# Kernel optimization log

Hardware: AMD Instinct MI355X
Metric: run time of the kernel (lower is better)

## Reference

```python
import jax, jax.numpy as jnp
import numpy as np
from jax import lax

WINDOW_SIZE = 11
SIGMA = 1.5
RGB_RANGE = 1.0
K1, K2 = 0.01, 0.03
CHANNELS = 3


def gaussian_window(window_size, sigma, channels, dtype=jnp.float32):
    coords = jnp.arange(window_size, dtype=dtype) - window_size // 2
    g = jnp.exp(-(coords ** 2) / (2.0 * sigma * sigma))
    g = g / g.sum()
    w2d = jnp.outer(g, g)
    w2d = w2d / w2d.sum()
    # depthwise kernel: (C, 1, ws, ws) in OIHW with feature_group_count=C
    return jnp.broadcast_to(w2d, (channels, 1, window_size, window_size)).astype(dtype)


def _dwconv(inp, window, padding):
    # depthwise conv2d, groups = C
    C = inp.shape[1]
    return lax.conv_general_dilated(
        inp, window,
        window_strides=(1, 1),
        padding=[(padding, padding), (padding, padding)],
        feature_group_count=C,
        dimension_numbers=('NCHW', 'OIHW', 'NCHW'))


def setup_inputs() -> dict:
    key = jax.random.key(0)
    kx, ky = jax.random.split(key)
    B, C, H, W = 16, CHANNELS, 512, 512
    x = jax.random.uniform(kx, (B, C, H, W), dtype=jnp.float32)
    y = jax.random.uniform(ky, (B, C, H, W), dtype=jnp.float32)
    window = gaussian_window(WINDOW_SIZE, SIGMA, C)
    return {"x": x, "y": y, "window": window}


def reference(x, y, window):
    padding = WINDOW_SIZE // 2
    mu_x = _dwconv(x, window, padding)
    mu_y = _dwconv(y, window, padding)
    mu_x2 = mu_x * mu_x
    mu_y2 = mu_y * mu_y
    mu_xy = mu_x * mu_y
    sigma_x2 = _dwconv(x * x, window, padding) - mu_x2
    sigma_y2 = _dwconv(y * y, window, padding) - mu_y2
    sigma_xy = _dwconv(x * y, window, padding) - mu_xy
    L = RGB_RANGE
    C1 = (K1 * L) ** 2
    C2 = (K2 * L) ** 2
    ssim_map = ((2.0 * mu_xy + C1) * (2.0 * sigma_xy + C2)) / (
        (mu_x2 + mu_y2 + C1) * (sigma_x2 + sigma_y2 + C2) + 1e-12)
    loss = 1.0 - ssim_map
    return loss.mean()
```

## Files before the change

kernel.cpp:

```cpp
#include <hip/hip_runtime.h>


typedef __fp16 f16x8 __attribute__((ext_vector_type(8)));
typedef float f32x4 __attribute__((ext_vector_type(4)));
typedef unsigned u32x4 __attribute__((ext_vector_type(4)));

__device__ __forceinline__ unsigned pk2(float a, float b) {
    return __builtin_bit_cast(unsigned, __builtin_amdgcn_cvt_pkrtz(a, b));
}
__device__ __forceinline__ f32x4 mfma16(f16x8 a, f16x8 b, f32x4 c) {
    return __builtin_amdgcn_mfma_f32_16x16x32_f16(a, b, c, 0, 0, 0);
}

#define SXW 24
#define HRP 40

__global__ __launch_bounds__(512, 8) void ssim_main(
    const float* __restrict__ xg, const float* __restrict__ yg,
    const float* __restrict__ w2d, float* __restrict__ part)
{
    __shared__ __align__(16) unsigned sx[80 * SXW];
    __shared__ __align__(16) unsigned sy[80 * SXW];
    __shared__ __align__(16) unsigned hq[2][32 * HRP];
    __shared__ unsigned tbp[64];
    __shared__ float gsf[12];
    __shared__ float wred[8];

    const int tid = threadIdx.x;

    if (tid < 12) {
        float s = 0.0f;
        if (tid < 11) {
            #pragma unroll
            for (int j = 0; j < 11; ++j) s += w2d[tid * 11 + j];
        }
        gsf[tid] = s;
    }

    const int nwg = 128 * (int)gridDim.z;
    const int flat = (int)blockIdx.x + 16 * ((int)blockIdx.y + 8 * (int)blockIdx.z);
    const int swz = (flat & 7) * (nwg >> 3) + (flat >> 3);
    const int bx = swz & 15, by = (swz >> 4) & 7, bz = swz >> 7;

    const int x0 = bx * 32 - 8;
    const int y0 = by * 64 - 9;
    const size_t zoff = (size_t)bz * (512 * 512);
    const float* __restrict__ xp = xg + zoff;
    const float* __restrict__ yp = yg + zoff;

    const bool interior = (x0 >= 0) & (x0 + 47 < 512) & (y0 >= 0) & (y0 + 79 < 512);
    if (interior) {
        for (int it = tid; it < 80 * 12; it += 512) {
            const int r = it / 12, c4 = it - r * 12;
            const int o = (y0 + r) * 512 + x0 + 4 * c4;
            const float4 vx = *(const float4*)&xp[o];
            const float4 vy = *(const float4*)&yp[o];
            *(uint2*)&sx[2 * it] = make_uint2(pk2(vx.x, vx.y), pk2(vx.z, vx.w));
            *(uint2*)&sy[2 * it] = make_uint2(pk2(vy.x, vy.y), pk2(vy.z, vy.w));
        }
    } else {
        for (int it = tid; it < 80 * 12; it += 512) {
            const int r = it / 12, c4 = it - r * 12;
            const int gr = y0 + r, gc0 = x0 + 4 * c4;
            const bool rok = (unsigned)gr < 512u;
            float xv[4], yv[4];
            #pragma unroll
            for (int j = 0; j < 4; ++j) {
                const int gc = gc0 + j;
                const bool ok = rok & ((unsigned)gc < 512u);
                const int o = gr * 512 + gc;
                xv[j] = ok ? xp[o] : 0.f;
                yv[j] = ok ? yp[o] : 0.f;
            }
            *(uint2*)&sx[2 * it] = make_uint2(pk2(xv[0], xv[1]), pk2(xv[2], xv[3]));
            *(uint2*)&sy[2 * it] = make_uint2(pk2(yv[0], yv[1]), pk2(yv[2], yv[3]));
        }
    }
    __syncthreads();

    if (tid < 64) {
        float ssum = 0.0f;
        #pragma unroll
        for (int k = 0; k < 11; ++k)
            if (k != 5) ssum += (float)(__fp16)gsf[k];
        const __fp16 cc = (__fp16)(1.0f - ssum);
        auto tap = [&](int t) -> __fp16 {
            if ((unsigned)t > 10u) return (__fp16)0.f;
            return (t == 5) ? cc : (__fp16)gsf[t];
        };
        const int t = tid - 19;
        const unsigned short lo = __builtin_bit_cast(unsigned short, tap(t));
        const unsigned short hi = __builtin_bit_cast(unsigned short, tap(t + 1));
        tbp[tid] = (unsigned)lo | ((unsigned)hi << 16);
    }
    __syncthreads();

    const int lane = tid & 63, wv = tid >> 6;
    const int lm = lane & 15, lg = lane >> 4;

    f16x8 bt, afr;
    {
        const int k0 = 8 * lg - lm + 16;
        u32x4 wb, wa;
        #pragma unroll
        for (int i = 0; i < 4; ++i) {
            wb[i] = tbp[k0 + 2 * i];
            wa[i] = tbp[k0 - 1 + 2 * i];
        }
        bt  = __builtin_bit_cast(f16x8, wb);
        afr = __builtin_bit_cast(f16x8, wa);
    }

    auto ldpair = [&](int i, f16x8& xa, f16x8& ya) {
        const int b = i >> 1, tl = i & 1;
        const int sbase = (16 * b + lm) * SXW + 8 * tl + 4 * lg;
        xa = __builtin_bit_cast(f16x8, *(const u32x4*)&sx[sbase]);
        ya = __builtin_bit_cast(f16x8, *(const u32x4*)&sy[sbase]);
    };
    f16x8 xa0, ya0;
    ldpair(wv, xa0, ya0);

    f32x4 acc[5];
    #pragma unroll
    for (int q = 0; q < 5; ++q) acc[q] = (f32x4){0.f, 0.f, 0.f, 0.f};

    const int rq = wv >> 1, ch = wv & 1;
    const int rpb = 8 * rq;

    #pragma unroll
    for (int chunk = 0; chunk < 3; ++chunk) {
        auto bitem = [&](const f16x8& xa, const f16x8& ya, int i) {
            const int b = i >> 1, tl = i & 1;
            const f32x4 z4 = {0.f, 0.f, 0.f, 0.f};
            f32x4 d0 = z4, d1 = z4;
            if (chunk == 0)      { d0 = mfma16(xa, bt, z4);      d1 = mfma16(ya, bt, z4); }
            else if (chunk == 1) { d0 = mfma16(xa * xa, bt, z4); d1 = mfma16(ya * ya, bt, z4); }
            else                 { d0 = mfma16(xa * ya, bt, z4); }
            const int ob = (16 * tl + lm) * HRP + 8 * b + 2 * lg;
            *(uint2*)&hq[0][ob] = make_uint2(pk2(d0[0], d0[1]), pk2(d0[2], d0[3]));
            if (chunk < 2)
                *(uint2*)&hq[1][ob] = make_uint2(pk2(d1[0], d1[1]), pk2(d1[2], d1[3]));
        };
        bitem(xa0, ya0, wv);
        if (wv < 2) {
            f16x8 xf, yf;
            ldpair(wv + 8, xf, yf);
            bitem(xf, yf, wv + 8);
        }
        __syncthreads();

        {
            const int cb = (16 * ch + lm) * HRP + rpb + 4 * lg;
            #pragma unroll
            for (int s = 0; s < 2; ++s) {
                if (chunk == 2 && s == 1) continue;
                const u32x4 w4 = *(const u32x4*)&hq[s][cb];
                acc[2 * chunk + s] =
                    mfma16(afr, __builtin_bit_cast(f16x8, w4), acc[2 * chunk + s]);
            }
        }
        if (chunk < 2) __syncthreads();
    }

    float lsum = 0.0f;
    const float C1 = 1e-4f, C2 = 9e-4f;
    #pragma unroll
    for (int r = 0; r < 4; ++r) {
        const float mx = acc[0][r], my = acc[1][r];
        const float exx = acc[2][r], eyy = acc[3][r];
        const float exy = acc[4][r];
        const float mx2 = mx * mx, my2 = my * my, mxy = mx * my;
        const float vx = exx - mx2, vy = eyy - my2, vxy = exy - mxy;
        const float num = (2.0f * mxy + C1) * (2.0f * vxy + C2);
        const float den = (mx2 + my2 + C1) * (vx + vy + C2) + 1e-12f;
        lsum = fmaf(num, __builtin_amdgcn_rcpf(den), lsum);
    }

    #pragma unroll
    for (int off = 32; off > 0; off >>= 1)
        lsum += __shfl_down(lsum, off, 64);
    if ((tid & 63) == 0) wred[tid >> 6] = lsum;
    __syncthreads();
    if (tid == 0) {
        float s = 0.0f;
        #pragma unroll
        for (int w = 0; w < 8; ++w) s += wred[w];
        part[swz] = s;
    }
}

__global__ __launch_bounds__(256) void ssim_reduce(
    const float* __restrict__ part, float* __restrict__ out,
    int n, float invN)
{
    __shared__ float wred[4];
    float s = 0.0f;
    for (int i = threadIdx.x; i < n; i += 256) s += part[i];
    #pragma unroll
    for (int off = 32; off > 0; off >>= 1)
        s += __shfl_down(s, off, 64);
    if ((threadIdx.x & 63) == 0) wred[threadIdx.x >> 6] = s;
    __syncthreads();
    if (threadIdx.x == 0)
        out[0] = 1.0f - (wred[0] + wred[1] + wred[2] + wred[3]) * invN;
}

extern "C" void kernel_launch(void* const* d_in, const int* in_sizes, int n_in,
                              void* d_out, int out_size, void* d_ws, size_t ws_size,
                              hipStream_t stream) {
    const float* x   = (const float*)d_in[0];
    const float* y   = (const float*)d_in[1];
    const float* w2d = (const float*)d_in[2];
    float* out  = (float*)d_out;
    float* part = (float*)d_ws;

    const int H = 512, W = 512;
    const int total = in_sizes[0];
    const int Z = total / (H * W);

    dim3 grid(W / 32, H / 64, Z);
    const int nblk = (W / 32) * (H / 64) * Z;
    ssim_main<<<grid, 512, 0, stream>>>(x, y, w2d, part);

    const float invN = 1.0f / (float)total;
    ssim_reduce<<<1, 256, 0, stream>>>(part, out, nblk, invN);
}
```

Measured before the change: 145.9 us.

## Process two tiles per workgroup with prefetch overlapping global loads and compute

Each workgroup now handles two adjacent 32x64 tiles, halving the grid. The second tile's global loads are issued into registers before the first tile's MFMA phases run, so memory latency overlaps compute. The five horizontal-pass results now go into five LDS buffers, which cuts the per-tile barriers from several chunked rounds to a few. Plain barriers are replaced with an explicit lgkmcnt wait plus s_barrier. In exchange, LDS use rises and the occupancy hint drops from 8 to 6, so fewer workgroups may be resident at once.

```diff
diff --git a/kernel.cpp b/kernel.cpp
--- a/kernel.cpp
+++ b/kernel.cpp
@@ -11,17 +11,20 @@
 __device__ __forceinline__ f32x4 mfma16(f16x8 a, f16x8 b, f32x4 c) {
     return __builtin_amdgcn_mfma_f32_16x16x32_f16(a, b, c, 0, 0, 0);
 }
+__device__ __forceinline__ void ldsBarrier() {
+    asm volatile("s_waitcnt lgkmcnt(0)\n\ts_barrier" ::: "memory");
+}
 
 #define SXW 24
 #define HRP 40
 
-__global__ __launch_bounds__(512, 8) void ssim_main(
+__global__ __launch_bounds__(512, 6) void ssim_main(
     const float* __restrict__ xg, const float* __restrict__ yg,
     const float* __restrict__ w2d, float* __restrict__ part)
 {
     __shared__ __align__(16) unsigned sx[80 * SXW];
     __shared__ __align__(16) unsigned sy[80 * SXW];
-    __shared__ __align__(16) unsigned hq[2][32 * HRP];
+    __shared__ __align__(16) unsigned hq[5][32 * HRP];
     __shared__ unsigned tbp[64];
     __shared__ float gsf[12];
     __shared__ float wred[8];
@@ -37,52 +40,64 @@
         gsf[tid] = s;
     }
 
-    const int nwg = 128 * (int)gridDim.z;
-    const int flat = (int)blockIdx.x + 16 * ((int)blockIdx.y + 8 * (int)blockIdx.z);
-    const int swz = (flat & 7) * (nwg >> 3) + (flat >> 3);
-    const int bx = swz & 15, by = (swz >> 4) & 7, bz = swz >> 7;
-
-    const int x0 = bx * 32 - 8;
-    const int y0 = by * 64 - 9;
-    const size_t zoff = (size_t)bz * (512 * 512);
-    const float* __restrict__ xp = xg + zoff;
-    const float* __restrict__ yp = yg + zoff;
-
-    const bool interior = (x0 >= 0) & (x0 + 47 < 512) & (y0 >= 0) & (y0 + 79 < 512);
-    if (interior) {
-        for (int it = tid; it < 80 * 12; it += 512) {
-            const int r = it / 12, c4 = it - r * 12;
+    const int npair = 64 * (int)gridDim.z;
+    const int flat = (int)blockIdx.x + 8 * ((int)blockIdx.y + 8 * (int)blockIdx.z);
+    const int k = (flat & 7) * (npair >> 3) + (flat >> 3);
+    const int t0 = 2 * k, t1 = 2 * k + 1;
+
+    const int it0 = tid, it1 = tid + 512;
+    const bool has1 = (it1 < 960);
+
+    auto decode = [&](int t, int& x0, int& y0, const float*& xp,
+                      const float*& yp, bool& inter) {
+        const int bx = t & 15, by = (t >> 4) & 7, bz = t >> 7;
+        x0 = bx * 32 - 8;
+        y0 = by * 64 - 9;
+        const size_t zoff = (size_t)bz * (512 * 512);
+        xp = xg + zoff; yp = yg + zoff;
+        inter = (x0 >= 0) & (x0 + 47 < 512) & (y0 >= 0) & (y0 + 79 < 512);
+    };
+    auto loadItem = [&](const float* xp, const float* yp, int x0, int y0,
+                        bool inter, int it, float4& xv, float4& yv) {
+        const int r = it / 12, c4 = it - r * 12;
+        if (inter) {
             const int o = (y0 + r) * 512 + x0 + 4 * c4;
-            const float4 vx = *(const float4*)&xp[o];
-            const float4 vy = *(const float4*)&yp[o];
-            *(uint2*)&sx[2 * it] = make_uint2(pk2(vx.x, vx.y), pk2(vx.z, vx.w));
-            *(uint2*)&sy[2 * it] = make_uint2(pk2(vy.x, vy.y), pk2(vy.z, vy.w));
-        }
-    } else {
-        for (int it = tid; it < 80 * 12; it += 512) {
-            const int r = it / 12, c4 = it - r * 12;
+            xv = *(const float4*)&xp[o];
+            yv = *(const float4*)&yp[o];
+        } else {
             const int gr = y0 + r, gc0 = x0 + 4 * c4;
             const bool rok = (unsigned)gr < 512u;
-            float xv[4], yv[4];
+            float tx[4], ty[4];
             #pragma unroll
             for (int j = 0; j < 4; ++j) {
                 const int gc = gc0 + j;
                 const bool ok = rok & ((unsigned)gc < 512u);
                 const int o = gr * 512 + gc;
-                xv[j] = ok ? xp[o] : 0.f;
-                yv[j] = ok ? yp[o] : 0.f;
+                tx[j] = ok ? xp[o] : 0.f;
+                ty[j] = ok ? yp[o] : 0.f;
             }
-            *(uint2*)&sx[2 * it] = make_uint2(pk2(xv[0], xv[1]), pk2(xv[2], xv[3]));
-            *(uint2*)&sy[2 * it] = make_uint2(pk2(yv[0], yv[1]), pk2(yv[2], yv[3]));
-        }
-    }
-    __syncthreads();
+            xv = make_float4(tx[0], tx[1], tx[2], tx[3]);
+            yv = make_float4(ty[0], ty[1], ty[2], ty[3]);
+        }
+    };
+    auto writeItem = [&](int it, const float4& xv, const float4& yv) {
+        *(uint2*)&sx[2 * it] = make_uint2(pk2(xv.x, xv.y), pk2(xv.z, xv.w));
+        *(uint2*)&sy[2 * it] = make_uint2(pk2(yv.x, yv.y), pk2(yv.z, yv.w));
+    };
+
+    int X0, Y0; const float *XP, *YP; bool I0;
+    decode(t0, X0, Y0, XP, YP, I0);
+    float4 ax0, ay0, ax1, ay1;
+    loadItem(XP, YP, X0, Y0, I0, it0, ax0, ay0);
+    if (has1) loadItem(XP, YP, X0, Y0, I0, it1, ax1, ay1);
+
+    ldsBarrier();
 
     if (tid < 64) {
         float ssum = 0.0f;
         #pragma unroll
-        for (int k = 0; k < 11; ++k)
-            if (k != 5) ssum += (float)(__fp16)gsf[k];
+        for (int kk = 0; kk < 11; ++kk)
+            if (kk != 5) ssum += (float)(__fp16)gsf[kk];
         const __fp16 cc = (__fp16)(1.0f - ssum);
         auto tap = [&](int t) -> __fp16 {
             if ((unsigned)t > 10u) return (__fp16)0.f;
@@ -93,7 +108,10 @@
         const unsigned short hi = __builtin_bit_cast(unsigned short, tap(t + 1));
         tbp[tid] = (unsigned)lo | ((unsigned)hi << 16);
     }
-    __syncthreads();
+
+    writeItem(it0, ax0, ay0);
+    if (has1) writeItem(it1, ax1, ay1);
+    ldsBarrier();
 
     const int lane = tid & 63, wv = tid >> 6;
     const int lm = lane & 15, lg = lane >> 4;
@@ -111,81 +129,82 @@
         afr = __builtin_bit_cast(f16x8, wa);
     }
 
-    auto ldpair = [&](int i, f16x8& xa, f16x8& ya) {
-        const int b = i >> 1, tl = i & 1;
-        const int sbase = (16 * b + lm) * SXW + 8 * tl + 4 * lg;
-        xa = __builtin_bit_cast(f16x8, *(const u32x4*)&sx[sbase]);
-        ya = __builtin_bit_cast(f16x8, *(const u32x4*)&sy[sbase]);
-    };
-    f16x8 xa0, ya0;
-    ldpair(wv, xa0, ya0);
-
-    f32x4 acc[5];
-    #pragma unroll
-    for (int q = 0; q < 5; ++q) acc[q] = (f32x4){0.f, 0.f, 0.f, 0.f};
-
     const int rq = wv >> 1, ch = wv & 1;
     const int rpb = 8 * rq;
-
-    #pragma unroll
-    for (int chunk = 0; chunk < 3; ++chunk) {
-        auto bitem = [&](const f16x8& xa, const f16x8& ya, int i) {
+    const f32x4 z4 = {0.f, 0.f, 0.f, 0.f};
+
+    auto phaseB = [&]() {
+        auto bitem = [&](int i) {
             const int b = i >> 1, tl = i & 1;
-            const f32x4 z4 = {0.f, 0.f, 0.f, 0.f};
-            f32x4 d0 = z4, d1 = z4;
-            if (chunk == 0)      { d0 = mfma16(xa, bt, z4);      d1 = mfma16(ya, bt, z4); }
-            else if (chunk == 1) { d0 = mfma16(xa * xa, bt, z4); d1 = mfma16(ya * ya, bt, z4); }
-            else                 { d0 = mfma16(xa * ya, bt, z4); }
+            const int sbase = (16 * b + lm) * SXW + 8 * tl + 4 * lg;
+            const f16x8 xa = __builtin_bit_cast(f16x8, *(const u32x4*)&sx[sbase]);
+            const f16x8 ya = __builtin_bit_cast(f16x8, *(const u32x4*)&sy[sbase]);
             const int ob = (16 * tl + lm) * HRP + 8 * b + 2 * lg;
-            *(uint2*)&hq[0][ob] = make_uint2(pk2(d0[0], d0[1]), pk2(d0[2], d0[3]));
-            if (chunk < 2)
-                *(uint2*)&hq[1][ob] = make_uint2(pk2(d1[0], d1[1]), pk2(d1[2], d1[3]));
+            f32x4 d;
+            d = mfma16(xa, bt, z4);
+            *(uint2*)&hq[0][ob] = make_uint2(pk2(d[0], d[1]), pk2(d[2], d[3]));
+            d = mfma16(ya, bt, z4);
+            *(uint2*)&hq[1][ob] = make_uint2(pk2(d[0], d[1]), pk2(d[2], d[3]));
+            d = mfma16(xa * xa, bt, z4);
+            *(uint2*)&hq[2][ob] = make_uint2(pk2(d[0], d[1]), pk2(d[2], d[3]));
+            d = mfma16(ya * ya, bt, z4);
+            *(uint2*)&hq[3][ob] = make_uint2(pk2(d[0], d[1]), pk2(d[2], d[3]));
+            d = mfma16(xa * ya, bt, z4);
+            *(uint2*)&hq[4][ob] = make_uint2(pk2(d[0], d[1]), pk2(d[2], d[3]));
         };
-        bitem(xa0, ya0, wv);
-        if (wv < 2) {
-            f16x8 xf, yf;
-            ldpair(wv + 8, xf, yf);
-            bitem(xf, yf, wv + 8);
-        }
-        __syncthreads();
-
-        {
-            const int cb = (16 * ch + lm) * HRP + rpb + 4 * lg;
-            #pragma unroll
-            for (int s = 0; s < 2; ++s) {
-                if (chunk == 2 && s == 1) continue;
-                const u32x4 w4 = *(const u32x4*)&hq[s][cb];
-                acc[2 * chunk + s] =
-                    mfma16(afr, __builtin_bit_cast(f16x8, w4), acc[2 * chunk + s]);
-            }
-        }
-        if (chunk < 2) __syncthreads();
-    }
-
-    float lsum = 0.0f;
-    const float C1 = 1e-4f, C2 = 9e-4f;
-    #pragma unroll
-    for (int r = 0; r < 4; ++r) {
-        const float mx = acc[0][r], my = acc[1][r];
-        const float exx = acc[2][r], eyy = acc[3][r];
-        const float exy = acc[4][r];
-        const float mx2 = mx * mx, my2 = my * my, mxy = mx * my;
-        const float vx = exx - mx2, vy = eyy - my2, vxy = exy - mxy;
-        const float num = (2.0f * mxy + C1) * (2.0f * vxy + C2);
-        const float den = (mx2 + my2 + C1) * (vx + vy + C2) + 1e-12f;
-        lsum = fmaf(num, __builtin_amdgcn_rcpf(den), lsum);
-    }
+        bitem(wv);
+        if (wv < 2) bitem(wv + 8);
+    };
+
+    auto phaseC = [&]() -> float {
+        const int cb = (16 * ch + lm) * HRP + rpb + 4 * lg;
+        f32x4 acc[5];
+        #pragma unroll
+        for (int q = 0; q < 5; ++q) {
+            const u32x4 w4 = *(const u32x4*)&hq[q][cb];
+            acc[q] = mfma16(afr, __builtin_bit_cast(f16x8, w4), z4);
+        }
+        float ls = 0.0f;
+        const float C1 = 1e-4f, C2 = 9e-4f;
+        #pragma unroll
+        for (int r = 0; r < 4; ++r) {
+            const float mx = acc[0][r], my = acc[1][r];
+            const float exx = acc[2][r], eyy = acc[3][r];
+            const float exy = acc[4][r];
+            const float mx2 = mx * mx, my2 = my * my, mxy = mx * my;
+            const float vx = exx - mx2, vy = eyy - my2, vxy = exy - mxy;
+            const float num = (2.0f * mxy + C1) * (2.0f * vxy + C2);
+            const float den = (mx2 + my2 + C1) * (vx + vy + C2) + 1e-12f;
+            ls = fmaf(num, __builtin_amdgcn_rcpf(den), ls);
+        }
+        return ls;
+    };
+
+    int X1, Y1; const float *XP1, *YP1; bool I1;
+    decode(t1, X1, Y1, XP1, YP1, I1);
+    loadItem(XP1, YP1, X1, Y1, I1, it0, ax0, ay0);
+    if (has1) loadItem(XP1, YP1, X1, Y1, I1, it1, ax1, ay1);
+
+    phaseB();
+    ldsBarrier();
+    float lsum = phaseC();
+    writeItem(it0, ax0, ay0);
+    if (has1) writeItem(it1, ax1, ay1);
+    ldsBarrier();
+    phaseB();
+    ldsBarrier();
+    lsum += phaseC();
 
     #pragma unroll
     for (int off = 32; off > 0; off >>= 1)
         lsum += __shfl_down(lsum, off, 64);
     if ((tid & 63) == 0) wred[tid >> 6] = lsum;
-    __syncthreads();
+    ldsBarrier();
     if (tid == 0) {
         float s = 0.0f;
         #pragma unroll
         for (int w = 0; w < 8; ++w) s += wred[w];
-        part[swz] = s;
+        part[k] = s;
     }
 }
 
@@ -218,10 +237,10 @@
     const int total = in_sizes[0];
     const int Z = total / (H * W);
 
-    dim3 grid(W / 32, H / 64, Z);
-    const int nblk = (W / 32) * (H / 64) * Z;
+    dim3 grid(W / 64, H / 64, Z);
+    const int npair = (W / 64) * (H / 64) * Z;
     ssim_main<<<grid, 512, 0, stream>>>(x, y, w2d, part);
 
     const float invN = 1.0f / (float)total;
-    ssim_reduce<<<1, 256, 0, stream>>>(part, out, nblk, invN);
-}
+    ssim_reduce<<<1, 256, 0, stream>>>(part, out, npair, invN);
+}
```

After: 143.0 us. 1.02x faster.

## Compute SSIM per-wave 16x16 tiles directly from global loads, dropping LDS staging

Applied to the files above, without the earlier changes.

Each wave now owns a 16x16 output tile and loads its 32x32 halo straight from global memory into MFMA operand registers, with no shared-memory input staging. The horizontal pass uses the 16x16x32 MFMA and the vertical pass uses two chained 16x16x16 MFMAs on packed fp16 results kept in registers, so the LDS round trip and block-wide barriers between passes go away. The block shrinks to 256 threads with four independent tiles, and the reduce kernel widens to handle the larger partial count. The cost is that neighbouring waves read overlapping halos, so more redundant global/L2 traffic (about 4x the input footprint versus roughly 1.9x before).

```diff
diff --git a/kernel.cpp b/kernel.cpp
--- a/kernel.cpp
+++ b/kernel.cpp
@@ -2,79 +2,36 @@
 
 
 typedef __fp16 f16x8 __attribute__((ext_vector_type(8)));
-typedef float f32x4 __attribute__((ext_vector_type(4)));
+typedef __fp16 f16x4 __attribute__((ext_vector_type(4)));
+typedef float  f32x4 __attribute__((ext_vector_type(4)));
+typedef unsigned u32x2 __attribute__((ext_vector_type(2)));
 typedef unsigned u32x4 __attribute__((ext_vector_type(4)));
 
 __device__ __forceinline__ unsigned pk2(float a, float b) {
     return __builtin_bit_cast(unsigned, __builtin_amdgcn_cvt_pkrtz(a, b));
 }
-__device__ __forceinline__ f32x4 mfma16(f16x8 a, f16x8 b, f32x4 c) {
+__device__ __forceinline__ f32x4 mfmaB(f16x8 a, f16x8 b, f32x4 c) {
     return __builtin_amdgcn_mfma_f32_16x16x32_f16(a, b, c, 0, 0, 0);
 }
+__device__ __forceinline__ f32x4 mfmaC(f16x4 a, f16x4 b, f32x4 c) {
+    return __builtin_amdgcn_mfma_f32_16x16x16f16(a, b, c, 0, 0, 0);
+}
 
-#define SXW 24
-#define HRP 40
-
-__global__ __launch_bounds__(512, 8) void ssim_main(
+__global__ __launch_bounds__(256, 6) void ssim_main(
     const float* __restrict__ xg, const float* __restrict__ yg,
     const float* __restrict__ w2d, float* __restrict__ part)
 {
-    __shared__ __align__(16) unsigned sx[80 * SXW];
-    __shared__ __align__(16) unsigned sy[80 * SXW];
-    __shared__ __align__(16) unsigned hq[2][32 * HRP];
+    __shared__ float gsf[11];
     __shared__ unsigned tbp[64];
-    __shared__ float gsf[12];
-    __shared__ float wred[8];
+    __shared__ float wred[4];
 
     const int tid = threadIdx.x;
 
-    if (tid < 12) {
+    if (tid < 11) {
         float s = 0.0f;
-        if (tid < 11) {
-            #pragma unroll
-            for (int j = 0; j < 11; ++j) s += w2d[tid * 11 + j];
-        }
+        #pragma unroll
+        for (int j = 0; j < 11; ++j) s += w2d[tid * 11 + j];
         gsf[tid] = s;
-    }
-
-    const int nwg = 128 * (int)gridDim.z;
-    const int flat = (int)blockIdx.x + 16 * ((int)blockIdx.y + 8 * (int)blockIdx.z);
-    const int swz = (flat & 7) * (nwg >> 3) + (flat >> 3);
-    const int bx = swz & 15, by = (swz >> 4) & 7, bz = swz >> 7;
-
-    const int x0 = bx * 32 - 8;
-    const int y0 = by * 64 - 9;
-    const size_t zoff = (size_t)bz * (512 * 512);
-    const float* __restrict__ xp = xg + zoff;
-    const float* __restrict__ yp = yg + zoff;
-
-    const bool interior = (x0 >= 0) & (x0 + 47 < 512) & (y0 >= 0) & (y0 + 79 < 512);
-    if (interior) {
-        for (int it = tid; it < 80 * 12; it += 512) {
-            const int r = it / 12, c4 = it - r * 12;
-            const int o = (y0 + r) * 512 + x0 + 4 * c4;
-            const float4 vx = *(const float4*)&xp[o];
-            const float4 vy = *(const float4*)&yp[o];
-            *(uint2*)&sx[2 * it] = make_uint2(pk2(vx.x, vx.y), pk2(vx.z, vx.w));
-            *(uint2*)&sy[2 * it] = make_uint2(pk2(vy.x, vy.y), pk2(vy.z, vy.w));
-        }
-    } else {
-        for (int it = tid; it < 80 * 12; it += 512) {
-            const int r = it / 12, c4 = it - r * 12;
-            const int gr = y0 + r, gc0 = x0 + 4 * c4;
-            const bool rok = (unsigned)gr < 512u;
-            float xv[4], yv[4];
-            #pragma unroll
-            for (int j = 0; j < 4; ++j) {
-                const int gc = gc0 + j;
-                const bool ok = rok & ((unsigned)gc < 512u);
-                const int o = gr * 512 + gc;
-                xv[j] = ok ? xp[o] : 0.f;
-                yv[j] = ok ? yp[o] : 0.f;
-            }
-            *(uint2*)&sx[2 * it] = make_uint2(pk2(xv[0], xv[1]), pk2(xv[2], xv[3]));
-            *(uint2*)&sy[2 * it] = make_uint2(pk2(yv[0], yv[1]), pk2(yv[2], yv[3]));
-        }
     }
     __syncthreads();
 
@@ -98,68 +55,73 @@
     const int lane = tid & 63, wv = tid >> 6;
     const int lm = lane & 15, lg = lane >> 4;
 
-    f16x8 bt, afr;
+    const int nblk = (int)gridDim.x;
+    const int bid = (int)blockIdx.x;
+    const int swz = (bid & 7) * (nblk >> 3) + (bid >> 3);
+    const int t = swz * 4 + wv;
+    const int tz = t >> 10, ty = (t >> 5) & 31, tx = t & 31;
+    const int x0 = 16 * tx - 8, y0 = 16 * ty - 8;
+    const bool border = (tx == 0) | (tx == 31) | (ty == 0) | (ty == 31);
+    const float* __restrict__ xp = xg + (size_t)tz * (512 * 512);
+    const float* __restrict__ yp = yg + (size_t)tz * (512 * 512);
+
+    auto ldband = [&](const float* __restrict__ p, int b) -> f16x8 {
+        const int gr = y0 + 16 * b + lm;
+        const int gc0 = x0 + 8 * lg;
+        u32x4 w;
+        if (!border) {
+            const float4 v0 = *(const float4*)&p[gr * 512 + gc0];
+            const float4 v1 = *(const float4*)&p[gr * 512 + gc0 + 4];
+            w = (u32x4){pk2(v0.x, v0.y), pk2(v0.z, v0.w),
+                        pk2(v1.x, v1.y), pk2(v1.z, v1.w)};
+        } else {
+            const bool rok = (unsigned)gr < 512u;
+            float v[8];
+            #pragma unroll
+            for (int j = 0; j < 8; ++j) {
+                const int gc = gc0 + j;
+                const bool ok = rok & ((unsigned)gc < 512u);
+                const int o = ok ? (gr * 512 + gc) : 0;
+                v[j] = ok ? p[o] : 0.f;
+            }
+            w = (u32x4){pk2(v[0], v[1]), pk2(v[2], v[3]),
+                        pk2(v[4], v[5]), pk2(v[6], v[7])};
+        }
+        return __builtin_bit_cast(f16x8, w);
+    };
+
+    const f16x8 xd0 = ldband(xp, 0), xd1 = ldband(xp, 1);
+    const f16x8 yd0 = ldband(yp, 0), yd1 = ldband(yp, 1);
+
+    f16x8 bt;
+    f16x4 ca0, ca1;
     {
-        const int k0 = 8 * lg - lm + 16;
-        u32x4 wb, wa;
-        #pragma unroll
-        for (int i = 0; i < 4; ++i) {
-            wb[i] = tbp[k0 + 2 * i];
-            wa[i] = tbp[k0 - 1 + 2 * i];
-        }
-        bt  = __builtin_bit_cast(f16x8, wb);
-        afr = __builtin_bit_cast(f16x8, wa);
+        const int ib = 8 * lg - lm + 16;
+        const u32x4 wb = {tbp[ib], tbp[ib + 2], tbp[ib + 4], tbp[ib + 6]};
+        bt = __builtin_bit_cast(f16x8, wb);
+        const int ic = 4 * lg - lm + 16;
+        const u32x2 w0 = {tbp[ic], tbp[ic + 2]};
+        const u32x2 w1 = {tbp[ic + 16], tbp[ic + 18]};
+        ca0 = __builtin_bit_cast(f16x4, w0);
+        ca1 = __builtin_bit_cast(f16x4, w1);
     }
 
-    auto ldpair = [&](int i, f16x8& xa, f16x8& ya) {
-        const int b = i >> 1, tl = i & 1;
-        const int sbase = (16 * b + lm) * SXW + 8 * tl + 4 * lg;
-        xa = __builtin_bit_cast(f16x8, *(const u32x4*)&sx[sbase]);
-        ya = __builtin_bit_cast(f16x8, *(const u32x4*)&sy[sbase]);
-    };
-    f16x8 xa0, ya0;
-    ldpair(wv, xa0, ya0);
-
+    const f32x4 z4 = {0.f, 0.f, 0.f, 0.f};
     f32x4 acc[5];
     #pragma unroll
-    for (int q = 0; q < 5; ++q) acc[q] = (f32x4){0.f, 0.f, 0.f, 0.f};
-
-    const int rq = wv >> 1, ch = wv & 1;
-    const int rpb = 8 * rq;
-
-    #pragma unroll
-    for (int chunk = 0; chunk < 3; ++chunk) {
-        auto bitem = [&](const f16x8& xa, const f16x8& ya, int i) {
-            const int b = i >> 1, tl = i & 1;
-            const f32x4 z4 = {0.f, 0.f, 0.f, 0.f};
-            f32x4 d0 = z4, d1 = z4;
-            if (chunk == 0)      { d0 = mfma16(xa, bt, z4);      d1 = mfma16(ya, bt, z4); }
-            else if (chunk == 1) { d0 = mfma16(xa * xa, bt, z4); d1 = mfma16(ya * ya, bt, z4); }
-            else                 { d0 = mfma16(xa * ya, bt, z4); }
-            const int ob = (16 * tl + lm) * HRP + 8 * b + 2 * lg;
-            *(uint2*)&hq[0][ob] = make_uint2(pk2(d0[0], d0[1]), pk2(d0[2], d0[3]));
-            if (chunk < 2)
-                *(uint2*)&hq[1][ob] = make_uint2(pk2(d1[0], d1[1]), pk2(d1[2], d1[3]));
-        };
-        bitem(xa0, ya0, wv);
-        if (wv < 2) {
-            f16x8 xf, yf;
-            ldpair(wv + 8, xf, yf);
-            bitem(xf, yf, wv + 8);
-        }
-        __syncthreads();
-
-        {
-            const int cb = (16 * ch + lm) * HRP + rpb + 4 * lg;
-            #pragma unroll
-            for (int s = 0; s < 2; ++s) {
-                if (chunk == 2 && s == 1) continue;
-                const u32x4 w4 = *(const u32x4*)&hq[s][cb];
-                acc[2 * chunk + s] =
-                    mfma16(afr, __builtin_bit_cast(f16x8, w4), acc[2 * chunk + s]);
-            }
-        }
-        if (chunk < 2) __syncthreads();
+    for (int q = 0; q < 5; ++q) {
+        f16x8 a0, a1;
+        if (q == 0)      { a0 = xd0;       a1 = xd1; }
+        else if (q == 1) { a0 = yd0;       a1 = yd1; }
+        else if (q == 2) { a0 = xd0 * xd0; a1 = xd1 * xd1; }
+        else if (q == 3) { a0 = yd0 * yd0; a1 = yd1 * yd1; }
+        else             { a0 = xd0 * yd0; a1 = xd1 * yd1; }
+        const f32x4 d0 = mfmaB(a0, bt, z4);
+        const f32x4 d1 = mfmaB(a1, bt, z4);
+        const u32x2 h0 = {pk2(d0[0], d0[1]), pk2(d0[2], d0[3])};
+        const u32x2 h1 = {pk2(d1[0], d1[1]), pk2(d1[2], d1[3])};
+        const f32x4 p0 = mfmaC(ca0, __builtin_bit_cast(f16x4, h0), z4);
+        acc[q]         = mfmaC(ca1, __builtin_bit_cast(f16x4, h1), p0);
     }
 
     float lsum = 0.0f;
@@ -181,28 +143,28 @@
         lsum += __shfl_down(lsum, off, 64);
     if ((tid & 63) == 0) wred[tid >> 6] = lsum;
     __syncthreads();
-    if (tid == 0) {
-        float s = 0.0f;
-        #pragma unroll
-        for (int w = 0; w < 8; ++w) s += wred[w];
-        part[swz] = s;
-    }
+    if (tid == 0)
+        part[bid] = wred[0] + wred[1] + wred[2] + wred[3];
 }
 
-__global__ __launch_bounds__(256) void ssim_reduce(
+__global__ __launch_bounds__(1024) void ssim_reduce(
     const float* __restrict__ part, float* __restrict__ out,
     int n, float invN)
 {
-    __shared__ float wred[4];
+    __shared__ float wred[16];
     float s = 0.0f;
-    for (int i = threadIdx.x; i < n; i += 256) s += part[i];
+    for (int i = threadIdx.x; i < n; i += 1024) s += part[i];
     #pragma unroll
     for (int off = 32; off > 0; off >>= 1)
         s += __shfl_down(s, off, 64);
     if ((threadIdx.x & 63) == 0) wred[threadIdx.x >> 6] = s;
     __syncthreads();
-    if (threadIdx.x == 0)
-        out[0] = 1.0f - (wred[0] + wred[1] + wred[2] + wred[3]) * invN;
+    if (threadIdx.x == 0) {
+        float tot = 0.0f;
+        #pragma unroll
+        for (int w = 0; w < 16; ++w) tot += wred[w];
+        out[0] = 1.0f - tot * invN;
+    }
 }
 
 extern "C" void kernel_launch(void* const* d_in, const int* in_sizes, int n_in,
@@ -218,10 +180,9 @@
     const int total = in_sizes[0];
     const int Z = total / (H * W);
 
-    dim3 grid(W / 32, H / 64, Z);
-    const int nblk = (W / 32) * (H / 64) * Z;
-    ssim_main<<<grid, 512, 0, stream>>>(x, y, w2d, part);
+    const int nblk = Z * 1024 / 4;
+    ssim_main<<<dim3(nblk), 256, 0, stream>>>(x, y, w2d, part);
 
     const float invN = 1.0f / (float)total;
-    ssim_reduce<<<1, 256, 0, stream>>>(part, out, nblk, invN);
+    ssim_reduce<<<1, 1024, 0, stream>>>(part, out, nblk, invN);
 }
```

Measured after the change: 162.3 us. 1.11x slower.
